# Kernel tuning notes

Measured on AMD Instinct MI355X. Metric: run time of the kernel, lower is better.

Reference implementation:

```python
import jax, jax.numpy as jnp
import numpy as np

N_HEADS, D_MODEL, D_HEAD = 16, 1024, 64
LN_EPS = 1e-5


def setup_inputs() -> dict:
    key = jax.random.key(0)
    ks = jax.random.split(key, 12)
    bs, s = 2, 2048
    hd = N_HEADS * D_HEAD
    sc = 0.02
    return {
        "q": jax.random.normal(ks[0], (bs, s, D_MODEL), jnp.float32),
        "kv": jax.random.normal(ks[1], (bs, s, D_MODEL), jnp.float32),
        "Wq": jax.random.normal(ks[2], (D_MODEL, hd), jnp.float32) * sc,
        "bq": jnp.zeros((hd,), jnp.float32),
        "Wk": jax.random.normal(ks[3], (D_MODEL, hd), jnp.float32) * sc,
        "bk": jnp.zeros((hd,), jnp.float32),
        "Wv": jax.random.normal(ks[4], (D_MODEL, hd), jnp.float32) * sc,
        "bv": jnp.zeros((hd,), jnp.float32),
        "Wo": jax.random.normal(ks[5], (hd, D_MODEL), jnp.float32) * sc,
        "bo": jnp.zeros((D_MODEL,), jnp.float32),
        "gamma": jnp.ones((D_MODEL,), jnp.float32),
        "beta": jnp.zeros((D_MODEL,), jnp.float32),
    }


def _split_heads(x):
    # [b, s, H*D] -> [b, H, s, D]
    b, s, _ = x.shape
    return x.reshape(b, s, N_HEADS, D_HEAD).transpose(0, 2, 1, 3)


def reference(q, kv, Wq, bq, Wk, bk, Wv, bv, Wo, bo, gamma, beta):
    wq = _split_heads(q @ Wq + bq)   # [b,H,Sq,D]
    wk = _split_heads(kv @ Wk + bk)  # [b,H,Sk,D]
    wv = _split_heads(kv @ Wv + bv)  # [b,H,Sk,D]
    scores = jnp.einsum("bhqd,bhkd->bhqk", wq, wk) / jnp.sqrt(
        jnp.asarray(D_HEAD, wq.dtype)
    )
    probs = jax.nn.softmax(scores, axis=-1)  # dropout p=0 -> identity
    attn = jnp.einsum("bhqk,bhkd->bhqd", probs, wv)
    b, _, sq, _ = attn.shape
    attn = attn.transpose(0, 2, 1, 3).reshape(b, sq, N_HEADS * D_HEAD)
    res = q + (attn @ Wo + bo)
    # LayerNorm over last dim
    mu = jnp.mean(res, axis=-1, keepdims=True)
    var = jnp.var(res, axis=-1, keepdims=True)
    return (res - mu) * jax.lax.rsqrt(var + LN_EPS) * gamma + beta
```

## Files before the change

kernel.cpp:

```cpp
#include <hip/hip_runtime.h>
#include <hip/hip_bf16.h>


#define DM 1024
#define SEQ 2048
#define NB 2
#define NH 16
#define DH 64

typedef __attribute__((ext_vector_type(8))) short bf16x8;
typedef __attribute__((ext_vector_type(4))) float f32x4;
typedef __attribute__((ext_vector_type(4))) unsigned int u32x4;

__device__ __forceinline__ float bf2f(short s) {
  unsigned u = ((unsigned)(unsigned short)s) << 16;
  return __builtin_bit_cast(float, u);
}
__device__ __forceinline__ short f2bf(float f) {
  unsigned u = __builtin_bit_cast(unsigned, f);
  u += 0x7fffu + ((u >> 16) & 1u);
  return (short)(u >> 16);
}
__device__ __forceinline__ unsigned cvt_pk_bf16(float lo, float hi) {
  unsigned r;
  asm("v_cvt_pk_bf16_f32 %0, %1, %2" : "=v"(r) : "v"(lo), "v"(hi));
  return r;
}
__device__ __forceinline__ float exp2_fast(float x) {
  float r;
  asm("v_exp_f32 %0, %1" : "=v"(r) : "v"(x));
  return r;
}

#define GLL16(gsrc, ldst)                                                     \
  __builtin_amdgcn_global_load_lds(                                           \
      (const __attribute__((address_space(1))) void*)(gsrc),                  \
      (__attribute__((address_space(3))) void*)(ldst), 16, 0, 0)

__global__ __launch_bounds__(256) void k_transpose(
    const float* __restrict__ Wq, const float* __restrict__ Wk,
    const float* __restrict__ Wv, const float* __restrict__ Wo,
    short* __restrict__ Wt_all) {
  const int z = blockIdx.z;
  const float* src = (z == 0) ? Wq : (z == 1) ? Wk : (z == 2) ? Wv : Wo;
  short* dst = Wt_all + (size_t)z * (DM * DM);
  __shared__ float t[32][33];
  const int n0 = blockIdx.x * 32, k0 = blockIdx.y * 32;
  const int tx = threadIdx.x, ty = threadIdx.y;
#pragma unroll
  for (int i = 0; i < 32; i += 8)
    t[ty + i][tx] = src[(size_t)(k0 + ty + i) * DM + n0 + tx];
  __syncthreads();
#pragma unroll
  for (int i = 0; i < 32; i += 8)
    dst[(size_t)(n0 + ty + i) * DM + k0 + tx] = f2bf(t[tx][ty + i]);
}

__global__ __launch_bounds__(256) void k_cvt(const float* __restrict__ q,
                                             const float* __restrict__ kv,
                                             short* __restrict__ qb,
                                             short* __restrict__ kvb) {
  const int i = blockIdx.x * 256 + threadIdx.x;
  const int half = 524288;
  const float* src = (i < half) ? q : kv;
  short* dst = (i < half) ? qb : kvb;
  const size_t j = (size_t)((i < half) ? i : i - half) * 8;
  const float4 a = *(const float4*)(src + j);
  const float4 b = *(const float4*)(src + j + 4);
  u32x4 pw;
  pw[0] = cvt_pk_bf16(a.x, a.y);
  pw[1] = cvt_pk_bf16(a.z, a.w);
  pw[2] = cvt_pk_bf16(b.x, b.y);
  pw[3] = cvt_pk_bf16(b.z, b.w);
  *(bf16x8*)(dst + j) = __builtin_bit_cast(bf16x8, pw);
}

__device__ __forceinline__ void gemm_body64(short* As, short* Bs,
                                            const short* __restrict__ X,
                                            const short* __restrict__ Wt,
                                            const float* __restrict__ bias,
                                            short* __restrict__ out,
                                            int vt_mode, float cscale,
                                            int bx, int by) {
  const int tid = threadIdx.x;
  const int w = tid >> 6, l = tid & 63;
  const int g = l >> 4, qi = l & 15;
  const int n0 = bx * 128;
  const int m0 = by * 128;
  const int wr = w >> 1, wc = w & 1;

  f32x4 acc[4][4];
#pragma unroll
  for (int m = 0; m < 4; m++)
#pragma unroll
    for (int n = 0; n < 4; n++) acc[m][n] = (f32x4){0.f, 0.f, 0.f, 0.f};

  const int srow = w * 8 + (l >> 3);
  const int scol = ((l & 7) ^ ((l >> 3) & 7)) * 8;
  const short* Ag = X + (size_t)(m0 + srow) * DM + scol;
  const short* Bg = Wt + (size_t)(n0 + srow) * DM + scol;

  for (int k0 = 0; k0 < DM; k0 += 64) {
    __syncthreads();
#pragma unroll
    for (int j = 0; j < 4; j++) {
      GLL16(Ag + (size_t)(j * 32) * DM + k0, As + j * 2048 + w * 512);
      GLL16(Bg + (size_t)(j * 32) * DM + k0, Bs + j * 2048 + w * 512);
    }
    __syncthreads();

#pragma unroll
    for (int kk = 0; kk < 2; kk++) {
      bf16x8 a[4], b[4];
#pragma unroll
      for (int m = 0; m < 4; m++)
        a[m] = *(const bf16x8*)&As[(wr * 64 + m * 16 + qi) * 64 +
                                   (((kk * 4 + g) ^ (qi & 7)) * 8)];
#pragma unroll
      for (int n = 0; n < 4; n++)
        b[n] = *(const bf16x8*)&Bs[(wc * 64 + n * 16 + qi) * 64 +
                                   (((kk * 4 + g) ^ (qi & 7)) * 8)];
#pragma unroll
      for (int m = 0; m < 4; m++)
#pragma unroll
        for (int n = 0; n < 4; n++)
          acc[m][n] = __builtin_amdgcn_mfma_f32_16x16x32_bf16(a[m], b[n],
                                                              acc[m][n], 0, 0, 0);
    }
  }

  const int col0 = n0 + wc * 64;
  const int row0 = m0 + wr * 64;
  float bfv[4];
#pragma unroll
  for (int n = 0; n < 4; n++) bfv[n] = bias[col0 + n * 16 + qi];

  if (!vt_mode) {
#pragma unroll
    for (int m = 0; m < 4; m++) {
#pragma unroll
      for (int n = 0; n < 4; n++) {
        const int col = col0 + n * 16 + qi;
#pragma unroll
        for (int r = 0; r < 4; r++) {
          const int row = row0 + m * 16 + g * 4 + r;
          out[(size_t)row * DM + col] = f2bf((acc[m][n][r] + bfv[n]) * cscale);
        }
      }
    }
  } else {
#pragma unroll
    for (int m = 0; m < 4; m++) {
      const int s_base = row0 + m * 16 + g * 4;
      const int bb = s_base >> 11;
      const int s = s_base & (SEQ - 1);
#pragma unroll
      for (int n = 0; n < 4; n++) {
        const int col = col0 + n * 16 + qi;
        const int h = col >> 6, d = col & 63;
        ushort4 v;
        v.x = (unsigned short)f2bf(acc[m][n][0] + bfv[n]);
        v.y = (unsigned short)f2bf(acc[m][n][1] + bfv[n]);
        v.z = (unsigned short)f2bf(acc[m][n][2] + bfv[n]);
        v.w = (unsigned short)f2bf(acc[m][n][3] + bfv[n]);
        *(ushort4*)&out[(((size_t)bb * NH + h) * DH + d) * SEQ + s] = v;
      }
    }
  }
}

__device__ __forceinline__ void xcd_remap(int& bx, int& by) {
  const int lin2 = blockIdx.x + 8 * blockIdx.y;
  const int xcd = lin2 & 7, jj = lin2 >> 3;
  bx = jj & 7;
  by = xcd * 4 + (jj >> 3);
}

__global__ __launch_bounds__(256) void k_gemm_qkv(
    const short* __restrict__ qb, const short* __restrict__ kvb,
    const short* __restrict__ Wt, const float* __restrict__ bq,
    const float* __restrict__ bk, const float* __restrict__ bv,
    short* __restrict__ qm, short* __restrict__ km, short* __restrict__ vtb) {
  __shared__ short As[8192], Bs[8192];
  const int z = blockIdx.z;
  const short* X = (z == 0) ? qb : kvb;
  const short* W = Wt + (size_t)z * (DM * DM);
  const float* bias = (z == 0) ? bq : (z == 1) ? bk : bv;
  short* out = (z == 0) ? qm : (z == 1) ? km : vtb;
  const float cs = (z == 0) ? 0.18033688011112042f : 1.0f;
  int bx, by;
  xcd_remap(bx, by);
  gemm_body64(As, Bs, X, W, bias, out, z == 2, cs, bx, by);
}

__global__ __launch_bounds__(256) void k_gemm_o(
    const short* __restrict__ attn, const short* __restrict__ Wto,
    const float* __restrict__ bo, short* __restrict__ om) {
  __shared__ short As[8192], Bs[8192];
  int bx, by;
  xcd_remap(bx, by);
  gemm_body64(As, Bs, attn, Wto, bo, om, 0, 1.0f, bx, by);
}

__global__ __launch_bounds__(256) void k_attn(const short* __restrict__ qm,
                                              const short* __restrict__ km,
                                              const short* __restrict__ vt,
                                              short* __restrict__ attn) {
  __shared__ short lds[2][8192];

  const int lin = blockIdx.x;
  const int xcd = lin & 7, j = lin >> 3;
  const int pair = xcd + 8 * (j >> 3);
  const int qb = j & 7;
  const int h = pair & 15, bb = pair >> 4;
  const int q0 = qb * 256;

  const int tid = threadIdx.x;
  const int w = tid >> 6, l = tid & 63;
  const int g = l >> 4, qi = l & 15;

  const size_t bbS = (size_t)bb * SEQ;
  const size_t vbase = ((size_t)(bb * NH + h)) * DH * SEQ;
  const short* __restrict__ kmh = km + bbS * DM + h * DH;

  const int skey = tid >> 3;
  const int sslot = tid & 7;
  const int kgq = sslot ^ ((skey >> 1) & 7);
  const int vkb = sslot ^ (skey & 7);
  const short* __restrict__ srcK0 = kmh + (size_t)skey * DM + kgq * 8;
  const short* __restrict__ srcV0 = vt + vbase + (size_t)skey * SEQ + vkb * 8;

#define STAGE(buf, kk0)                                                       \
  {                                                                           \
    GLL16(srcK0 + (size_t)(kk0)*DM, &lds[buf][w * 512]);                      \
    GLL16(srcK0 + (size_t)((kk0) + 32) * DM, &lds[buf][2048 + w * 512]);      \
    GLL16(srcV0 + (kk0), &lds[buf][4096 + w * 512]);                          \
    GLL16(srcV0 + (kk0) + 32 * (size_t)SEQ, &lds[buf][6144 + w * 512]);       \
  }

  const int rowA = q0 + w * 64 + qi;
  const short* Qp = qm + (bbS + rowA) * DM + h * DH;
  const bf16x8 qA0 = *(const bf16x8*)(Qp + 8 * g);
  const bf16x8 qA1 = *(const bf16x8*)(Qp + 32 + 8 * g);
  const bf16x8 qB0 = *(const bf16x8*)(Qp + 16 * DM + 8 * g);
  const bf16x8 qB1 = *(const bf16x8*)(Qp + 16 * DM + 32 + 8 * g);
  const bf16x8 qC0 = *(const bf16x8*)(Qp + 32 * DM + 8 * g);
  const bf16x8 qC1 = *(const bf16x8*)(Qp + 32 * DM + 32 + 8 * g);
  const bf16x8 qD0 = *(const bf16x8*)(Qp + 48 * DM + 8 * g);
  const bf16x8 qD1 = *(const bf16x8*)(Qp + 48 * DM + 32 + 8 * g);

  float ssA[4], ssB[4], ssC[4], ssD[4];
#pragma unroll
  for (int i = 0; i < 4; i++) { ssA[i] = 0.f; ssB[i] = 0.f; ssC[i] = 0.f; ssD[i] = 0.f; }
  f32x4 oA[4], oB[4], oC[4], oD[4];
#pragma unroll
  for (int f = 0; f < 4; f++) {
    oA[f] = (f32x4){0.f, 0.f, 0.f, 0.f};
    oB[f] = (f32x4){0.f, 0.f, 0.f, 0.f};
    oC[f] = (f32x4){0.f, 0.f, 0.f, 0.f};
    oD[f] = (f32x4){0.f, 0.f, 0.f, 0.f};
  }

  const int xA = (g ^ (qi & 7)) * 8;
  const int xB = ((4 + g) ^ (qi & 7)) * 8;

#define SM_PACK(S0, S1, SS, PB)                                               \
  bf16x8 PB;                                                                  \
  {                                                                           \
    float e0_[4], e1_[4];                                                     \
    _Pragma("unroll") for (int r = 0; r < 4; r++) {                           \
      e0_[r] = exp2_fast(S0[r]);                                              \
      e1_[r] = exp2_fast(S1[r]);                                              \
      SS[r] += e0_[r] + e1_[r];                                               \
    }                                                                         \
    u32x4 pw_;                                                                \
    _Pragma("unroll") for (int r = 0; r < 4; r++)                             \
        pw_[r] = cvt_pk_bf16(e0_[r], e1_[r]);                                 \
    PB = __builtin_bit_cast(bf16x8, pw_);                                     \
  }

  auto tile = [&](const short* Ks, const short* Vs) {
#pragma unroll
    for (int s = 0; s < 2; s++) {
      const int r0 = (32 * s + 2 * qi) * 64;
      const bf16x8 k00 = *(const bf16x8*)&Ks[r0 + xA];
      const bf16x8 k01 = *(const bf16x8*)&Ks[r0 + xB];
      const bf16x8 k10 = *(const bf16x8*)&Ks[r0 + 64 + xA];
      const bf16x8 k11 = *(const bf16x8*)&Ks[r0 + 64 + xB];

      f32x4 sA0 = (f32x4){0.f, 0.f, 0.f, 0.f}, sA1 = sA0;
      f32x4 sB0 = sA0, sB1 = sA0, sC0 = sA0, sC1 = sA0, sD0 = sA0, sD1 = sA0;
      __builtin_amdgcn_s_setprio(1);
      sA0 = __builtin_amdgcn_mfma_f32_16x16x32_bf16(k00, qA0, sA0, 0, 0, 0);
      sA0 = __builtin_amdgcn_mfma_f32_16x16x32_bf16(k01, qA1, sA0, 0, 0, 0);
      sA1 = __builtin_amdgcn_mfma_f32_16x16x32_bf16(k10, qA0, sA1, 0, 0, 0);
      sA1 = __builtin_amdgcn_mfma_f32_16x16x32_bf16(k11, qA1, sA1, 0, 0, 0);
      sB0 = __builtin_amdgcn_mfma_f32_16x16x32_bf16(k00, qB0, sB0, 0, 0, 0);
      sB0 = __builtin_amdgcn_mfma_f32_16x16x32_bf16(k01, qB1, sB0, 0, 0, 0);
      sB1 = __builtin_amdgcn_mfma_f32_16x16x32_bf16(k10, qB0, sB1, 0, 0, 0);
      sB1 = __builtin_amdgcn_mfma_f32_16x16x32_bf16(k11, qB1, sB1, 0, 0, 0);
      sC0 = __builtin_amdgcn_mfma_f32_16x16x32_bf16(k00, qC0, sC0, 0, 0, 0);
      sC0 = __builtin_amdgcn_mfma_f32_16x16x32_bf16(k01, qC1, sC0, 0, 0, 0);
      sC1 = __builtin_amdgcn_mfma_f32_16x16x32_bf16(k10, qC0, sC1, 0, 0, 0);
      sC1 = __builtin_amdgcn_mfma_f32_16x16x32_bf16(k11, qC1, sC1, 0, 0, 0);
      sD0 = __builtin_amdgcn_mfma_f32_16x16x32_bf16(k00, qD0, sD0, 0, 0, 0);
      sD0 = __builtin_amdgcn_mfma_f32_16x16x32_bf16(k01, qD1, sD0, 0, 0, 0);
      sD1 = __builtin_amdgcn_mfma_f32_16x16x32_bf16(k10, qD0, sD1, 0, 0, 0);
      sD1 = __builtin_amdgcn_mfma_f32_16x16x32_bf16(k11, qD1, sD1, 0, 0, 0);
      __builtin_amdgcn_s_setprio(0);

      SM_PACK(sA0, sA1, ssA, pbA)
      SM_PACK(sB0, sB1, ssB, pbB)
      SM_PACK(sC0, sC1, ssC, pbC)
      SM_PACK(sD0, sD1, ssD, pbD)

      const int vx = ((4 * s + g) ^ (qi & 7)) * 8;
      __builtin_amdgcn_s_setprio(1);
#pragma unroll
      for (int f = 0; f < 4; f++) {
        const bf16x8 vv = *(const bf16x8*)&Vs[(qi + 16 * f) * 64 + vx];
        oA[f] = __builtin_amdgcn_mfma_f32_16x16x32_bf16(vv, pbA, oA[f], 0, 0, 0);
        oB[f] = __builtin_amdgcn_mfma_f32_16x16x32_bf16(vv, pbB, oB[f], 0, 0, 0);
        oC[f] = __builtin_amdgcn_mfma_f32_16x16x32_bf16(vv, pbC, oC[f], 0, 0, 0);
        oD[f] = __builtin_amdgcn_mfma_f32_16x16x32_bf16(vv, pbD, oD[f], 0, 0, 0);
      }
      __builtin_amdgcn_s_setprio(0);
    }
  };

  STAGE(0, 0);
  for (int t = 0; t < 32; ++t) {
    __syncthreads();
    if (t < 31) STAGE((t + 1) & 1, (t + 1) * 64);
    tile(&lds[t & 1][0], &lds[t & 1][4096]);
  }

#define WRITE_G(SS, O, ROWOFF)                                                \
  {                                                                           \
    float ss_ = (SS[0] + SS[1]) + (SS[2] + SS[3]);                            \
    ss_ += __shfl_xor(ss_, 16);                                               \
    ss_ += __shfl_xor(ss_, 32);                                               \
    const float inv_ = 1.f / ss_;                                             \
    short* Op_ = attn + (bbS + rowA + (ROWOFF)) * DM + h * DH;                \
    _Pragma("unroll") for (int f = 0; f < 4; f++) {                           \
      ushort4 v_;                                                             \
      v_.x = (unsigned short)f2bf(O[f][0] * inv_);                            \
      v_.y = (unsigned short)f2bf(O[f][1] * inv_);                            \
      v_.z = (unsigned short)f2bf(O[f][2] * inv_);                            \
      v_.w = (unsigned short)f2bf(O[f][3] * inv_);                            \
      *(ushort4*)(Op_ + f * 16 + g * 4) = v_;                                 \
    }                                                                         \
  }

  WRITE_G(ssA, oA, 0)
  WRITE_G(ssB, oB, 16)
  WRITE_G(ssC, oC, 32)
  WRITE_G(ssD, oD, 48)
#undef STAGE
#undef SM_PACK
#undef WRITE_G
}

__global__ __launch_bounds__(256) void k_ln(const float* __restrict__ q,
                                            const short* __restrict__ om,
                                            const float* __restrict__ gamma,
                                            const float* __restrict__ beta,
                                            float* __restrict__ out) {
  const int row = blockIdx.x;
  const int t = threadIdx.x;
  const int w = t >> 6, l = t & 63;
  const size_t base = (size_t)row * DM + t * 4;
  const float4 qv = *(const float4*)(q + base);
  const ushort4 ov = *(const ushort4*)(om + base);
  float v[4];
  v[0] = qv.x + bf2f((short)ov.x);
  v[1] = qv.y + bf2f((short)ov.y);
  v[2] = qv.z + bf2f((short)ov.z);
  v[3] = qv.w + bf2f((short)ov.w);
  float s = v[0] + v[1] + v[2] + v[3];
  float s2 = v[0] * v[0] + v[1] * v[1] + v[2] * v[2] + v[3] * v[3];
#pragma unroll
  for (int off = 32; off >= 1; off >>= 1) {
    s += __shfl_xor(s, off);
    s2 += __shfl_xor(s2, off);
  }
  __shared__ float ps[4], ps2[4];
  if (l == 0) {
    ps[w] = s;
    ps2[w] = s2;
  }
  __syncthreads();
  const float St = ps[0] + ps[1] + ps[2] + ps[3];
  const float S2t = ps2[0] + ps2[1] + ps2[2] + ps2[3];
  const float mu = St * (1.f / 1024.f);
  float var = S2t * (1.f / 1024.f) - mu * mu;
  const float rstd = rsqrtf(var + 1e-5f);
  const float4 gv = *(const float4*)(gamma + t * 4);
  const float4 bv = *(const float4*)(beta + t * 4);
  float4 ovv;
  ovv.x = (v[0] - mu) * rstd * gv.x + bv.x;
  ovv.y = (v[1] - mu) * rstd * gv.y + bv.y;
  ovv.z = (v[2] - mu) * rstd * gv.z + bv.z;
  ovv.w = (v[3] - mu) * rstd * gv.w + bv.w;
  *(float4*)(out + base) = ovv;
}

extern "C" void kernel_launch(void* const* d_in, const int* in_sizes, int n_in,
                              void* d_out, int out_size, void* d_ws, size_t ws_size,
                              hipStream_t stream) {
  const float* q = (const float*)d_in[0];
  const float* kv = (const float*)d_in[1];
  const float* Wq = (const float*)d_in[2];
  const float* bq = (const float*)d_in[3];
  const float* Wk = (const float*)d_in[4];
  const float* bk = (const float*)d_in[5];
  const float* Wv = (const float*)d_in[6];
  const float* bv = (const float*)d_in[7];
  const float* Wo = (const float*)d_in[8];
  const float* bo = (const float*)d_in[9];
  const float* gamma = (const float*)d_in[10];
  const float* beta = (const float*)d_in[11];

  short* ws = (short*)d_ws;
  short* Wt = ws;
  short* qb16 = ws + 4u * 1048576u;
  short* kvb16 = qb16 + 4194304u;
  short* qm = kvb16 + 4194304u;
  short* km = qm + 4194304u;
  short* vtb = km + 4194304u;
  short* attnb = qb16;
  short* om = kvb16;

  hipLaunchKernelGGL(k_transpose, dim3(32, 32, 4), dim3(32, 8), 0, stream,
                     Wq, Wk, Wv, Wo, Wt);
  hipLaunchKernelGGL(k_cvt, dim3(4096), dim3(256), 0, stream, q, kv, qb16, kvb16);
  hipLaunchKernelGGL(k_gemm_qkv, dim3(8, 32, 3), dim3(256), 0, stream,
                     qb16, kvb16, Wt, bq, bk, bv, qm, km, vtb);
  hipLaunchKernelGGL(k_attn, dim3(256), dim3(256), 0, stream,
                     qm, km, vtb, attnb);
  hipLaunchKernelGGL(k_gemm_o, dim3(8, 32, 1), dim3(256), 0, stream,
                     attnb, Wt + 3u * 1048576u, bo, om);
  hipLaunchKernelGGL(k_ln, dim3(4096), dim3(256), 0, stream,
                     q, om, gamma, beta, (float*)d_out);
}
```

Before: 131.0 us.

## Double-buffer GEMM K-loop with BK=32 and split attention into 128-query blocks

```diff
diff --git a/kernel.cpp b/kernel.cpp
--- a/kernel.cpp
+++ b/kernel.cpp
@@ -75,7 +75,7 @@
   *(bf16x8*)(dst + j) = __builtin_bit_cast(bf16x8, pw);
 }
 
-__device__ __forceinline__ void gemm_body64(short* As, short* Bs,
+__device__ __forceinline__ void gemm_body32(short (*As)[4096], short (*Bs)[4096],
                                             const short* __restrict__ X,
                                             const short* __restrict__ Wt,
                                             const float* __restrict__ bias,
@@ -95,38 +95,43 @@
 #pragma unroll
     for (int n = 0; n < 4; n++) acc[m][n] = (f32x4){0.f, 0.f, 0.f, 0.f};
 
-  const int srow = w * 8 + (l >> 3);
-  const int scol = ((l & 7) ^ ((l >> 3) & 7)) * 8;
+  const int srow = w * 16 + (l >> 2);
+  const int scol = ((l & 3) ^ ((l >> 2) & 3)) * 8;
   const short* Ag = X + (size_t)(m0 + srow) * DM + scol;
   const short* Bg = Wt + (size_t)(n0 + srow) * DM + scol;
 
-  for (int k0 = 0; k0 < DM; k0 += 64) {
+  auto stage = [&](int buf, int k0) {
+#pragma unroll
+    for (int jj = 0; jj < 2; ++jj) {
+      GLL16(Ag + (size_t)(jj * 64) * DM + k0, &As[buf][jj * 2048 + w * 512]);
+      GLL16(Bg + (size_t)(jj * 64) * DM + k0, &Bs[buf][jj * 2048 + w * 512]);
+    }
+  };
+
+  auto compute = [&](int buf) {
+    bf16x8 a[4], b[4];
+    const int xo = (g ^ (qi & 3)) * 8;
+#pragma unroll
+    for (int m = 0; m < 4; m++)
+      a[m] = *(const bf16x8*)&As[buf][(wr * 64 + m * 16 + qi) * 32 + xo];
+#pragma unroll
+    for (int n = 0; n < 4; n++)
+      b[n] = *(const bf16x8*)&Bs[buf][(wc * 64 + n * 16 + qi) * 32 + xo];
+    __builtin_amdgcn_s_setprio(1);
+#pragma unroll
+    for (int m = 0; m < 4; m++)
+#pragma unroll
+      for (int n = 0; n < 4; n++)
+        acc[m][n] = __builtin_amdgcn_mfma_f32_16x16x32_bf16(a[m], b[n],
+                                                            acc[m][n], 0, 0, 0);
+    __builtin_amdgcn_s_setprio(0);
+  };
+
+  stage(0, 0);
+  for (int ks = 0; ks < 32; ++ks) {
     __syncthreads();
-#pragma unroll
-    for (int j = 0; j < 4; j++) {
-      GLL16(Ag + (size_t)(j * 32) * DM + k0, As + j * 2048 + w * 512);
-      GLL16(Bg + (size_t)(j * 32) * DM + k0, Bs + j * 2048 + w * 512);
-    }
-    __syncthreads();
-
-#pragma unroll
-    for (int kk = 0; kk < 2; kk++) {
-      bf16x8 a[4], b[4];
-#pragma unroll
-      for (int m = 0; m < 4; m++)
-        a[m] = *(const bf16x8*)&As[(wr * 64 + m * 16 + qi) * 64 +
-                                   (((kk * 4 + g) ^ (qi & 7)) * 8)];
-#pragma unroll
-      for (int n = 0; n < 4; n++)
-        b[n] = *(const bf16x8*)&Bs[(wc * 64 + n * 16 + qi) * 64 +
-                                   (((kk * 4 + g) ^ (qi & 7)) * 8)];
-#pragma unroll
-      for (int m = 0; m < 4; m++)
-#pragma unroll
-        for (int n = 0; n < 4; n++)
-          acc[m][n] = __builtin_amdgcn_mfma_f32_16x16x32_bf16(a[m], b[n],
-                                                              acc[m][n], 0, 0, 0);
-    }
+    if (ks < 31) stage((ks + 1) & 1, (ks + 1) * 32);
+    compute(ks & 1);
   }
 
   const int col0 = n0 + wc * 64;
@@ -181,7 +186,7 @@
     const short* __restrict__ Wt, const float* __restrict__ bq,
     const float* __restrict__ bk, const float* __restrict__ bv,
     short* __restrict__ qm, short* __restrict__ km, short* __restrict__ vtb) {
-  __shared__ short As[8192], Bs[8192];
+  __shared__ short As[2][4096], Bs[2][4096];
   const int z = blockIdx.z;
   const short* X = (z == 0) ? qb : kvb;
   const short* W = Wt + (size_t)z * (DM * DM);
@@ -190,19 +195,19 @@
   const float cs = (z == 0) ? 0.18033688011112042f : 1.0f;
   int bx, by;
   xcd_remap(bx, by);
-  gemm_body64(As, Bs, X, W, bias, out, z == 2, cs, bx, by);
+  gemm_body32(As, Bs, X, W, bias, out, z == 2, cs, bx, by);
 }
 
 __global__ __launch_bounds__(256) void k_gemm_o(
     const short* __restrict__ attn, const short* __restrict__ Wto,
     const float* __restrict__ bo, short* __restrict__ om) {
-  __shared__ short As[8192], Bs[8192];
+  __shared__ short As[2][4096], Bs[2][4096];
   int bx, by;
   xcd_remap(bx, by);
-  gemm_body64(As, Bs, attn, Wto, bo, om, 0, 1.0f, bx, by);
-}
-
-__global__ __launch_bounds__(256) void k_attn(const short* __restrict__ qm,
+  gemm_body32(As, Bs, attn, Wto, bo, om, 0, 1.0f, bx, by);
+}
+
+__global__ __launch_bounds__(128) void k_attn(const short* __restrict__ qm,
                                               const short* __restrict__ km,
                                               const short* __restrict__ vt,
                                               short* __restrict__ attn) {
@@ -210,10 +215,10 @@
 
   const int lin = blockIdx.x;
   const int xcd = lin & 7, j = lin >> 3;
-  const int pair = xcd + 8 * (j >> 3);
-  const int qb = j & 7;
+  const int pair = xcd + 8 * (j >> 4);
+  const int qb = j & 15;
   const int h = pair & 15, bb = pair >> 4;
-  const int q0 = qb * 256;
+  const int q0 = qb * 128;
 
   const int tid = threadIdx.x;
   const int w = tid >> 6, l = tid & 63;
@@ -232,10 +237,12 @@
 
 #define STAGE(buf, kk0)                                                       \
   {                                                                           \
-    GLL16(srcK0 + (size_t)(kk0)*DM, &lds[buf][w * 512]);                      \
-    GLL16(srcK0 + (size_t)((kk0) + 32) * DM, &lds[buf][2048 + w * 512]);      \
-    GLL16(srcV0 + (kk0), &lds[buf][4096 + w * 512]);                          \
-    GLL16(srcV0 + (kk0) + 32 * (size_t)SEQ, &lds[buf][6144 + w * 512]);       \
+    _Pragma("unroll") for (int jj = 0; jj < 4; ++jj)                          \
+        GLL16(srcK0 + (size_t)((kk0) + 16 * jj) * DM,                         \
+              &lds[buf][jj * 1024 + w * 512]);                                \
+    _Pragma("unroll") for (int jj = 0; jj < 4; ++jj)                          \
+        GLL16(srcV0 + (kk0) + (size_t)(16 * jj) * SEQ,                        \
+              &lds[buf][4096 + jj * 1024 + w * 512]);                         \
   }
 
   const int rowA = q0 + w * 64 + qi;
@@ -436,7 +443,7 @@
   hipLaunchKernelGGL(k_cvt, dim3(4096), dim3(256), 0, stream, q, kv, qb16, kvb16);
   hipLaunchKernelGGL(k_gemm_qkv, dim3(8, 32, 3), dim3(256), 0, stream,
                      qb16, kvb16, Wt, bq, bk, bv, qm, km, vtb);
-  hipLaunchKernelGGL(k_attn, dim3(256), dim3(256), 0, stream,
+  hipLaunchKernelGGL(k_attn, dim3(512), dim3(128), 0, stream,
                      qm, km, vtb, attnb);
   hipLaunchKernelGGL(k_gemm_o, dim3(8, 32, 1), dim3(256), 0, stream,
                      attnb, Wt + 3u * 1048576u, bo, om);
```

Measured after the change: 163.9 us. 1.25x slower.
